# Performance work log

Measured on AMD Instinct MI355X. Metric: run time of the kernel, lower is better.

The kernel has to match this reference:

```python
import jax, jax.numpy as jnp
import numpy as np

B, T = 2, 1024
D_MODEL = 2048
D_STATE = 64            # N
HEADDIM = 64            # P (module sets headdim = d_state)
EXPAND = 2
D_CONV = 4
NGROUPS = 1
D_INNER = EXPAND * D_MODEL                     # 4096
NHEADS = D_INNER // HEADDIM                    # 64
CONV_DIM = D_INNER + 2 * NGROUPS * D_STATE     # 4224
D_IN_PROJ = 2 * D_INNER + 2 * NGROUPS * D_STATE + NHEADS  # 8384
EPS = 1e-5


def setup_inputs() -> dict:
    key = jax.random.key(0)
    k = jax.random.split(key, 10)
    n = lambda kk, sh, sc: jax.random.normal(kk, sh, jnp.float32) * sc
    return {
        "x": n(k[0], (B, T, D_MODEL), 1.0),
        "ln_w": jnp.ones((D_MODEL,), jnp.float32),
        "ln_b": jnp.zeros((D_MODEL,), jnp.float32),
        "in_proj_w": n(k[1], (D_IN_PROJ, D_MODEL), D_MODEL ** -0.5),
        "conv_w": n(k[2], (CONV_DIM, D_CONV), 0.5),
        "conv_b": n(k[3], (CONV_DIM,), 0.02),
        "dt_bias": n(k[4], (NHEADS,), 0.5),
        "A_log": jnp.log(jax.random.uniform(k[5], (NHEADS,), jnp.float32, 1.0, 16.0)),
        "D": 1.0 + n(k[6], (NHEADS,), 0.1),
        "norm_w": jnp.ones((D_INNER,), jnp.float32),
        "out_proj_w": n(k[7], (D_MODEL, D_INNER), D_INNER ** -0.5),
    }


def _layernorm(x, w, b):
    mu = x.mean(-1, keepdims=True)
    var = ((x - mu) ** 2).mean(-1, keepdims=True)
    return (x - mu) * jax.lax.rsqrt(var + EPS) * w + b


def _mamba2(u, in_proj_w, conv_w, conv_b, dt_bias, A_log, D, norm_w, out_proj_w):
    zxbcdt = u @ in_proj_w.T                         # [B,T,D_IN_PROJ]
    z = zxbcdt[..., :D_INNER]                        # gate
    xBC = zxbcdt[..., D_INNER:D_INNER + CONV_DIM]
    dt = zxbcdt[..., D_INNER + CONV_DIM:]            # [B,T,H]
    # causal depthwise conv1d (kernel size D_CONV) + SiLU
    xp = jnp.pad(xBC, ((0, 0), (D_CONV - 1, 0), (0, 0)))
    conv = conv_b
    for kk in range(D_CONV):
        conv = conv + xp[:, kk:kk + T, :] * conv_w[:, kk]
    xBC = jax.nn.silu(conv)
    x_in = xBC[..., :D_INNER].reshape(B, T, NHEADS, HEADDIM)   # [B,T,H,P]
    Bm = xBC[..., D_INNER:D_INNER + D_STATE]         # [B,T,N] (ngroups=1)
    Cm = xBC[..., D_INNER + D_STATE:]                # [B,T,N]
    dt = jax.nn.softplus(dt + dt_bias)               # [B,T,H]
    A = -jnp.exp(A_log)                              # [H]
    dA = jnp.exp(dt * A)                             # [B,T,H]
    dtx = dt[..., None] * x_in                       # [B,T,H,P]

    def step(h, inp):
        dA_t, dtx_t, B_t, C_t = inp
        # h: [B,H,P,N]
        h = h * dA_t[:, :, None, None] + dtx_t[..., None] * B_t[:, None, None, :]
        y = jnp.einsum('bhpn,bn->bhp', h, C_t)
        return h, y

    h0 = jnp.zeros((B, NHEADS, HEADDIM, D_STATE), u.dtype)
    xs = (jnp.moveaxis(dA, 1, 0), jnp.moveaxis(dtx, 1, 0),
          jnp.moveaxis(Bm, 1, 0), jnp.moveaxis(Cm, 1, 0))
    _, ys = jax.lax.scan(step, h0, xs)               # ys: [T,B,H,P]
    y = jnp.moveaxis(ys, 0, 1) + D[:, None] * x_in   # skip term D*x
    y = y.reshape(B, T, D_INNER)
    # gated RMSNorm (norm_before_gate=False): rmsnorm(y * silu(z)) * w
    y = y * jax.nn.silu(z)
    y = y * jax.lax.rsqrt((y * y).mean(-1, keepdims=True) + EPS) * norm_w
    return y @ out_proj_w.T                          # [B,T,D_MODEL]


def reference(x, ln_w, ln_b, in_proj_w, conv_w, conv_b, dt_bias, A_log, D, norm_w, out_proj_w):
    # pre-norm Mamba2 block with residual: x + Mamba2(LayerNorm(x))
    return x + _mamba2(_layernorm(x, ln_w, ln_b), in_proj_w, conv_w, conv_b,
                       dt_bias, A_log, D, norm_w, out_proj_w)
```

## Files before the change

### kernel.cpp

```cpp
#include <hip/hip_runtime.h>
#include <hip/hip_bf16.h>

#define Bdim 2
#define Tdim 1024
#define DMODEL 2048
#define DSTATE 64
#define HEADDIM 64
#define DCONV 4
#define DINNER 4096
#define NHEADS 64
#define CONVDIM 4224
#define DINPROJ 8384
#define NPAD 8448
#define MROWS (Bdim*Tdim)
#define QC 64
#define NCHUNK (Tdim/QC)

typedef __attribute__((ext_vector_type(8))) short bf16x8;
typedef __attribute__((ext_vector_type(4))) float f32x4;
typedef __attribute__((ext_vector_type(4))) unsigned short u16x4;
typedef __attribute__((ext_vector_type(8))) unsigned short u16x8;

#define GLB(p) ((const __attribute__((address_space(1))) void*)(p))
#define LDS(p) ((__attribute__((address_space(3))) void*)(p))

__device__ __forceinline__ unsigned short f2bf(float f) {
    unsigned int x = __builtin_bit_cast(unsigned int, f);
    x += 0x7fffu + ((x >> 16) & 1u);
    return (unsigned short)(x >> 16);
}
__device__ __forceinline__ float bf2f(unsigned int u16) {
    unsigned int x = u16 << 16;
    return __builtin_bit_cast(float, x);
}
__device__ __forceinline__ float siluf(float v) {
    return v / (1.f + expf(-v));
}

#define CVT_A4 (NPAD * DMODEL / 4)
#define CVT_B4 (DMODEL * DINNER / 4)
#define CVT_BLKS ((CVT_A4 + CVT_B4) / 256)
__global__ __launch_bounds__(256) void prep_k(const float* __restrict__ in_proj,
                                              const float* __restrict__ out_proj,
                                              unsigned short* __restrict__ win,
                                              unsigned short* __restrict__ wout,
                                              const float* __restrict__ x,
                                              const float* __restrict__ lw,
                                              const float* __restrict__ lb,
                                              unsigned short* __restrict__ u) {
    if (blockIdx.x < CVT_BLKS) {
        int idx = blockIdx.x * 256 + threadIdx.x;
        if (idx < CVT_A4) {
            int i4 = idx * 4;
            int row = i4 >> 11;
            u16x4 o;
            if (row < DINPROJ) {
                float4 v = *(const float4*)(in_proj + i4);
                o = (u16x4){f2bf(v.x), f2bf(v.y), f2bf(v.z), f2bf(v.w)};
            } else {
                o = (u16x4){0, 0, 0, 0};
            }
            *(u16x4*)(win + i4) = o;
        } else {
            int i4 = (idx - CVT_A4) * 4;
            float4 v = *(const float4*)(out_proj + i4);
            *(u16x4*)(wout + i4) = (u16x4){f2bf(v.x), f2bf(v.y), f2bf(v.z), f2bf(v.w)};
        }
        return;
    }
    int row = blockIdx.x - CVT_BLKS;
    const float* xr = x + (size_t)row * DMODEL;
    float4 v[2];
    float s = 0.f, s2 = 0.f;
#pragma unroll
    for (int i = 0; i < 2; ++i) {
        int c = (threadIdx.x + 256 * i) * 4;
        v[i] = *(const float4*)(xr + c);
        s += v[i].x + v[i].y + v[i].z + v[i].w;
        s2 += v[i].x * v[i].x + v[i].y * v[i].y + v[i].z * v[i].z + v[i].w * v[i].w;
    }
#pragma unroll
    for (int off = 32; off; off >>= 1) { s += __shfl_down(s, off); s2 += __shfl_down(s2, off); }
    __shared__ float rs[4], rs2[4];
    if ((threadIdx.x & 63) == 0) { rs[threadIdx.x >> 6] = s; rs2[threadIdx.x >> 6] = s2; }
    __syncthreads();
    s = rs[0] + rs[1] + rs[2] + rs[3];
    s2 = rs2[0] + rs2[1] + rs2[2] + rs2[3];
    float mu = s * (1.f / DMODEL);
    float var = s2 * (1.f / DMODEL) - mu * mu;
    float inv = rsqrtf(var + 1e-5f);
#pragma unroll
    for (int i = 0; i < 2; ++i) {
        int c = (threadIdx.x + 256 * i) * 4;
        float4 wv = *(const float4*)(lw + c);
        float4 bv = *(const float4*)(lb + c);
        u16x4 o = {f2bf((v[i].x - mu) * inv * wv.x + bv.x),
                   f2bf((v[i].y - mu) * inv * wv.y + bv.y),
                   f2bf((v[i].z - mu) * inv * wv.z + bv.z),
                   f2bf((v[i].w - mu) * inv * wv.w + bv.w)};
        *(u16x4*)(u + (size_t)row * DMODEL + c) = o;
    }
}

#define WAITV(n) asm volatile("s_waitcnt vmcnt(" #n ")" ::: "memory")
#define LGKM0   do { asm volatile("s_waitcnt lgkmcnt(0)" ::: "memory"); \
                     __builtin_amdgcn_sched_barrier(0); } while (0)
#define SCB     __builtin_amdgcn_sched_barrier(0)
#define BAR     __builtin_amdgcn_s_barrier()

template <int KTILES>
__global__ __launch_bounds__(512, 2) void gemm8(const unsigned short* __restrict__ A,
                                                const unsigned short* __restrict__ Bw,
                                                float* __restrict__ Cout,
                                                int N, int lda, int ldb,
                                                int nb, int mb) {
    __shared__ unsigned short As[2][256 * 64];
    __shared__ unsigned short Bs[2][128 * 64];

    const int bid = blockIdx.x;
    const int per_panel = mb * 8;
    const int fullp = (nb / 8) * per_panel;
    int mt, nt;
    if (bid < fullp) {
        int p = bid / per_panel, r = bid % per_panel;
        nt = p * 8 + r / mb; mt = r % mb;
    } else {
        int r = bid - fullp;
        nt = (nb / 8) * 8 + r / mb; mt = r % mb;
    }
    const int m0 = mt * 256, n0 = nt * 128;

    const int tid = threadIdx.x;
    const int lane = tid & 63, w = tid >> 6;
    const int wm = (w >> 1) * 64;
    const int wn = (w & 1) * 64;
    const int row16 = lane & 15, quad = lane >> 4;
    const int swz = row16 & 7;

    const unsigned short* gA[4];
    const unsigned short* gB[2];
#pragma unroll
    for (int l = 0; l < 4; ++l) {
        int c = l * 512 + tid, r = c >> 3, kb = (c & 7) ^ (r & 7);
        gA[l] = A + (size_t)(m0 + r) * lda + kb * 8;
    }
#pragma unroll
    for (int l = 0; l < 2; ++l) {
        int c = l * 512 + tid, r = c >> 3, kb = (c & 7) ^ (r & 7);
        gB[l] = Bw + (size_t)(n0 + r) * ldb + kb * 8;
    }

#define STG_A(d, l, kt) __builtin_amdgcn_global_load_lds(GLB(gA[l] + (kt) * 64), \
                            LDS(&As[d][((l) * 512 + tid) * 8]), 16, 0, 0)
#define STG_B(d, l, kt) __builtin_amdgcn_global_load_lds(GLB(gB[l] + (kt) * 64), \
                            LDS(&Bs[d][((l) * 512 + tid) * 8]), 16, 0, 0)
#define RD_B(d) _Pragma("unroll") for (int j = 0; j < 4; ++j)                      \
                _Pragma("unroll") for (int kc = 0; kc < 2; ++kc) {                 \
                    int row = wn + j * 16 + row16;                                 \
                    int g = (kc * 4 + quad) ^ swz;                                 \
                    bfr[j][kc] = *(const bf16x8*)&Bs[d][(row * 8 + g) * 8];        \
                }
#define RD_A(d, ms) _Pragma("unroll") for (int i2 = 0; i2 < 2; ++i2)               \
                    _Pragma("unroll") for (int kc = 0; kc < 2; ++kc) {             \
                        int row = wm + ((ms) * 2 + i2) * 16 + row16;               \
                        int g = (kc * 4 + quad) ^ swz;                             \
                        af[i2][kc] = *(const bf16x8*)&As[d][(row * 8 + g) * 8];    \
                    }
#define MM(ms) do { __builtin_amdgcn_s_setprio(1);                                  \
                    _Pragma("unroll") for (int kc = 0; kc < 2; ++kc)                \
                    _Pragma("unroll") for (int i2 = 0; i2 < 2; ++i2)                \
                    _Pragma("unroll") for (int j = 0; j < 4; ++j)                   \
                        acc[(ms) * 2 + i2][j] = __builtin_amdgcn_mfma_f32_16x16x32_bf16( \
                            af[i2][kc], bfr[j][kc], acc[(ms) * 2 + i2][j], 0, 0, 0);\
                    __builtin_amdgcn_s_setprio(0); } while (0)

    f32x4 acc[4][4];
#pragma unroll
    for (int i = 0; i < 4; ++i)
#pragma unroll
        for (int j = 0; j < 4; ++j) acc[i][j] = (f32x4){0.f, 0.f, 0.f, 0.f};
    bf16x8 bfr[4][2], af[2][2];

    STG_A(0, 0, 0); STG_A(0, 1, 0); STG_A(0, 2, 0); STG_A(0, 3, 0);
    STG_B(0, 0, 0); STG_B(0, 1, 0);

    const int KI = KTILES / 2;
    for (int i = 0; i < KI; ++i) {
        const int k1 = 2 * i + 1, k2 = 2 * i + 2;
        const bool st2 = (k2 < KTILES);
        STG_A(1, 0, k1); STG_A(1, 1, k1); STG_A(1, 2, k1); STG_A(1, 3, k1);
        WAITV(4);
        BAR;
        RD_B(0); RD_A(0, 0);
        LGKM0;
        MM(0);
        BAR;
        RD_A(0, 1);
        STG_B(1, 0, k1); STG_B(1, 1, k1);
        BAR;
        LGKM0;
        MM(1);
        BAR;
        if (st2) {
            STG_A(0, 0, k2); STG_A(0, 1, k2); STG_A(0, 2, k2); STG_A(0, 3, k2);
            WAITV(4);
        } else {
            WAITV(0);
        }
        BAR;
        RD_B(1); RD_A(1, 0);
        LGKM0;
        MM(0);
        BAR;
        RD_A(1, 1);
        if (st2) { STG_B(0, 0, k2); STG_B(0, 1, k2); }
        BAR;
        LGKM0;
        MM(1);
        BAR;
    }

#pragma unroll
    for (int i2 = 0; i2 < 4; ++i2)
#pragma unroll
        for (int j = 0; j < 4; ++j)
#pragma unroll
            for (int r = 0; r < 4; ++r) {
                int m = m0 + wm + i2 * 16 + quad * 4 + r;
                int n = n0 + wn + j * 16 + row16;
                Cout[(size_t)m * N + n] = acc[i2][j][r];
            }
#undef STG_A
#undef STG_B
#undef RD_A
#undef RD_B
#undef MM
}

template <int EPI, int BM, int BN, int KTILES>
__global__ __launch_bounds__(512, 1) void gemm_mf(const unsigned short* __restrict__ A,
                                                  const unsigned short* __restrict__ Bw,
                                                  float* __restrict__ Cout,
                                                  const float* __restrict__ resid,
                                                  int N, int lda, int ldb,
                                                  int nb, int mb) {
    constexpr int NA = BM / 64;
    constexpr int NB = BN / 64;
    constexpr int IM = BM / 64;
    constexpr int IMH = IM / 2;
    constexpr int IN = BN / 32;

    __shared__ unsigned short As[3][BM * 64];
    __shared__ unsigned short Bs[3][BN * 64];

    const int bid = blockIdx.x;
    const int per_panel = mb * 8;
    const int fullp = (nb / 8) * per_panel;
    int mt, nt;
    if (bid < fullp) {
        int p = bid / per_panel, r = bid % per_panel;
        nt = p * 8 + r / mb; mt = r % mb;
    } else {
        int r = bid - fullp;
        nt = (nb / 8) * 8 + r / mb; mt = r % mb;
    }
    const int m0 = mt * BM, n0 = nt * BN;

    const int tid = threadIdx.x;
    const int lane = tid & 63, w = tid >> 6;
    const int wm = (w >> 1) * (BM / 4);
    const int wn = (w & 1) * 64;
    const int row16 = lane & 15, quad = lane >> 4;
    const int swz = row16 & 7;

    const unsigned short* gA[NA]; int oA[NA];
    const unsigned short* gB[NB]; int oB[NB];
#pragma unroll
    for (int l = 0; l < NA; ++l) {
        int c = l * 512 + tid, r = c >> 3, kb = (c & 7) ^ (r & 7);
        gA[l] = A + (size_t)(m0 + r) * lda + kb * 8;
        oA[l] = c * 8;
    }
#pragma unroll
    for (int l = 0; l < NB; ++l) {
        int c = l * 512 + tid, r = c >> 3, kb = (c & 7) ^ (r & 7);
        gB[l] = Bw + (size_t)(n0 + r) * ldb + kb * 8;
        oB[l] = c * 8;
    }

#define STG_A(d, kt) do { _Pragma("unroll")                                           \
    for (int _l = 0; _l < NA; ++_l)                                                   \
        __builtin_amdgcn_global_load_lds(GLB(gA[_l] + (kt) * 64),                     \
                                         LDS(&As[d][oA[_l]]), 16, 0, 0); } while (0)
#define STG_B(d, kt) do { _Pragma("unroll")                                           \
    for (int _l = 0; _l < NB; ++_l)                                                   \
        __builtin_amdgcn_global_load_lds(GLB(gB[_l] + (kt) * 64),                     \
                                         LDS(&Bs[d][oB[_l]]), 16, 0, 0); } while (0)
#define RD_B(Bb) do { _Pragma("unroll") for (int _j = 0; _j < IN; ++_j)               \
                      _Pragma("unroll") for (int _kc = 0; _kc < 2; ++_kc) {           \
                          int _row = wn + _j * 16 + row16;                            \
                          int _g = (_kc * 4 + quad) ^ swz;                            \
                          bfr[_j][_kc] = *(const bf16x8*)&(Bb)[(_row * 8 + _g) * 8];  \
                      } } while (0)
#define RD_A(Ab, h) do { _Pragma("unroll") for (int _i = 0; _i < IMH; ++_i)           \
                         _Pragma("unroll") for (int _kc = 0; _kc < 2; ++_kc) {        \
                             int _row = wm + ((h) * IMH + _i) * 16 + row16;           \
                             int _g = (_kc * 4 + quad) ^ swz;                         \
                             af[_i][_kc] = *(const bf16x8*)&(Ab)[(_row * 8 + _g) * 8];\
                         } } while (0)
#define MM(h) do { __builtin_amdgcn_s_setprio(1);                                     \
                   _Pragma("unroll") for (int _kc = 0; _kc < 2; ++_kc)                \
                   _Pragma("unroll") for (int _i = 0; _i < IMH; ++_i)                 \
                   _Pragma("unroll") for (int _j = 0; _j < IN; ++_j)                  \
                       acc[(h) * IMH + _i][_j] = __builtin_amdgcn_mfma_f32_16x16x32_bf16( \
                           af[_i][_kc], bfr[_j][_kc], acc[(h) * IMH + _i][_j], 0, 0, 0);  \
                   __builtin_amdgcn_s_setprio(0); } while (0)

    f32x4 acc[IM][IN];
#pragma unroll
    for (int i = 0; i < IM; ++i)
#pragma unroll
        for (int j = 0; j < IN; ++j) acc[i][j] = (f32x4){0.f, 0.f, 0.f, 0.f};
    bf16x8 bfr[IN][2], af[IMH][2];

    STG_A(0, 0); STG_B(0, 0);
    STG_A(1, 1); STG_B(1, 1);
    if constexpr (BM == 256) WAITV(6); else WAITV(4);
    BAR;

    int bc = 0;
    for (int t = 0; t < KTILES; ++t) {
        int bn2 = bc + 2; if (bn2 >= 3) bn2 -= 3;
        const unsigned short* Ab = As[bc];
        const unsigned short* Bb = Bs[bc];
        const bool pf = (t + 2 < KTILES);

        RD_B(Bb); RD_A(Ab, 0);
        if (pf) STG_A(bn2, t + 2);
        SCB;
        BAR;
        LGKM0;
        MM(0);
        BAR;
        RD_A(Ab, 1);
        if (pf) STG_B(bn2, t + 2);
        SCB;
        if (t + 2 < KTILES) { if constexpr (BM == 256) WAITV(6); else WAITV(4); }
        else if (t + 1 < KTILES) WAITV(0);
        BAR;
        LGKM0;
        MM(1);
        BAR;
        bc = bc + 1; if (bc == 3) bc = 0;
    }

#pragma unroll
    for (int i = 0; i < IM; ++i)
#pragma unroll
        for (int j = 0; j < IN; ++j)
#pragma unroll
            for (int r = 0; r < 4; ++r) {
                int m = m0 + wm + i * 16 + quad * 4 + r;
                int n = n0 + wn + j * 16 + row16;
                float v = acc[i][j][r];
                if (EPI == 0)
                    Cout[(size_t)m * N + n] = v;
                else
                    Cout[(size_t)m * N + n] = resid[(size_t)m * N + n] + v;
            }
#undef STG_A
#undef STG_B
#undef RD_A
#undef RD_B
#undef MM
}

#define CONV_T (MROWS * CONVDIM / 4)
__global__ __launch_bounds__(256) void convdt_k(const float* __restrict__ zx,
                                                const float* __restrict__ cw,
                                                const float* __restrict__ cb,
                                                const float* __restrict__ dt_bias,
                                                const float* __restrict__ A_log,
                                                float* __restrict__ xin,
                                                float* __restrict__ bcf,
                                                float* __restrict__ dtf,
                                                float* __restrict__ dtAf) {
    int idx = blockIdx.x * 256 + threadIdx.x;
    if (idx < CONV_T) {
        int cg = idx % (CONVDIM / 4);
        int bt = idx / (CONVDIM / 4);
        int c = cg * 4;
        int t = bt & (Tdim - 1);
        const float* base = zx + (size_t)bt * NPAD + DINNER + c;
        float4 acc = *(const float4*)(cb + c);
#pragma unroll
        for (int kk = 0; kk < DCONV; ++kk) {
            int tt = t - 3 + kk;
            if (tt >= 0) {
                float4 v = *(const float4*)(base + (long)(kk - 3) * NPAD);
                acc.x += v.x * cw[(c + 0) * 4 + kk];
                acc.y += v.y * cw[(c + 1) * 4 + kk];
                acc.z += v.z * cw[(c + 2) * 4 + kk];
                acc.w += v.w * cw[(c + 3) * 4 + kk];
            }
        }
        float4 s = {siluf(acc.x), siluf(acc.y), siluf(acc.z), siluf(acc.w)};
        if (c < DINNER) *(float4*)(xin + (size_t)bt * DINNER + c) = s;
        else            *(float4*)(bcf + (size_t)bt * 128 + (c - DINNER)) = s;
    } else {
        int d4 = (idx - CONV_T) * 4;
        int bt = d4 >> 6;
        int h = d4 & 63;
        float4 raw = *(const float4*)(zx + (size_t)bt * NPAD + (DINNER + CONVDIM) + h);
        float4 bias = *(const float4*)(dt_bias + h);
        float4 al = *(const float4*)(A_log + h);
        float r[4] = {raw.x + bias.x, raw.y + bias.y, raw.z + bias.z, raw.w + bias.w};
        float A[4] = {-expf(al.x), -expf(al.y), -expf(al.z), -expf(al.w)};
        float4 dtv, dta;
        float* dtp = (float*)&dtv; float* dap = (float*)&dta;
#pragma unroll
        for (int j = 0; j < 4; ++j) {
            float dv = (r[j] > 20.f) ? r[j] : log1pf(expf(r[j]));
            dtp[j] = dv;
            dap[j] = dv * A[j];
        }
        *(float4*)(dtf + bt * 64 + h) = dtv;
        *(float4*)(dtAf + bt * 64 + h) = dta;
    }
}

__global__ __launch_bounds__(256) void chunk_state_k(const float* __restrict__ xin,
                                                     const float* __restrict__ bcf,
                                                     const float* __restrict__ dtf,
                                                     const float* __restrict__ dtAf,
                                                     float* __restrict__ Sst,
                                                     float* __restrict__ laq) {
    const int blk = blockIdx.x;
    const int c = blk & 15, h = (blk >> 4) & 63, b = blk >> 10;
    const int bt0 = b * Tdim + c * QC;
    const int tid = threadIdx.x;

    __shared__ float Bs[QC][68];
    __shared__ float Dx[QC][68];
    __shared__ float wsh[QC];

    if (tid < QC) {
        float v = dtAf[(bt0 + tid) * NHEADS + h];
#pragma unroll
        for (int d = 1; d < 64; d <<= 1) {
            float o = __shfl_up(v, d, 64);
            v += (tid >= d) ? o : 0.f;
        }
        float la63 = __shfl(v, 63, 64);
        wsh[tid] = expf(la63 - v);
        if (tid == 63) laq[blk] = la63;
    }
    __syncthreads();

    const int row = tid >> 2, q = tid & 3;
    {
        float m = wsh[row] * dtf[(bt0 + row) * NHEADS + h];
        const float* xr = xin + (size_t)(bt0 + row) * DINNER + h * 64 + q * 16;
        const float* br = bcf + (size_t)(bt0 + row) * 128 + q * 16;
#pragma unroll
        for (int j = 0; j < 4; ++j) {
            float4 xv = *(const float4*)(xr + j * 4);
            float4 bv = *(const float4*)(br + j * 4);
            *(float4*)&Dx[row][q * 16 + j * 4] = (float4){m * xv.x, m * xv.y, m * xv.z, m * xv.w};
            *(float4*)&Bs[row][q * 16 + j * 4] = bv;
        }
    }
    __syncthreads();

    const int p0 = (tid >> 4) * 4, n0 = (tid & 15) * 4;
    float acc[4][4] = {};
    for (int i = 0; i < QC; ++i) {
        float4 dv = *(const float4*)&Dx[i][p0];
        float4 bv = *(const float4*)&Bs[i][n0];
        float dva[4] = {dv.x, dv.y, dv.z, dv.w};
        float bva[4] = {bv.x, bv.y, bv.z, bv.w};
#pragma unroll
        for (int a = 0; a < 4; ++a)
#pragma unroll
            for (int e = 0; e < 4; ++e) acc[a][e] += dva[a] * bva[e];
    }
    float* Sp = Sst + (size_t)blk * NPAD;
#pragma unroll
    for (int a = 0; a < 4; ++a)
        *(float4*)&Sp[(p0 + a) * 64 + n0] = (float4){acc[a][0], acc[a][1], acc[a][2], acc[a][3]};
}

__global__ __launch_bounds__(256) void combine_k(float* __restrict__ Sst,
                                                 const float* __restrict__ laq) {
    const int bh = blockIdx.x >> 1;
    const int half = blockIdx.x & 1;
    const int tid = threadIdx.x;
    float4 r0 = {}, r1 = {};
    for (int c = 0; c < NCHUNK - 1; ++c) {
        float* p = Sst + (size_t)(bh * 16 + c) * NPAD + half * 2048 + tid * 8;
        float P = expf(laq[bh * 16 + c]);
        float4 s0 = ((const float4*)p)[0], s1 = ((const float4*)p)[1];
        r0 = (float4){P * r0.x + s0.x, P * r0.y + s0.y, P * r0.z + s0.z, P * r0.w + s0.w};
        r1 = (float4){P * r1.x + s1.x, P * r1.y + s1.y, P * r1.z + s1.z, P * r1.w + s1.w};
        ((float4*)p)[0] = r0; ((float4*)p)[1] = r1;
    }
}

__global__ __launch_bounds__(256) void chunk_out_k2(float* __restrict__ xin,
                                                    const float* __restrict__ bcf,
                                                    const float* __restrict__ dtf,
                                                    const float* __restrict__ dtAf,
                                                    const float* __restrict__ Sst,
                                                    const float* __restrict__ Dp) {
    const int blk = blockIdx.x;
    const int c = blk & 15, h = (blk >> 4) & 63, b = blk >> 10;
    const int bt0 = b * Tdim + c * QC;
    const int tid = threadIdx.x;

    __shared__ unsigned short Csh[64 * 64];
    __shared__ unsigned short Bsh[64 * 64];
    __shared__ unsigned short DxT[64 * 64];
    __shared__ unsigned short Gh [64 * 64];
    __shared__ unsigned short Hh [64 * 64];
    __shared__ float lash[QC];

    if (tid < QC) {
        float v = dtAf[(bt0 + tid) * NHEADS + h];
#pragma unroll
        for (int d = 1; d < 64; d <<= 1) {
            float o = __shfl_up(v, d, 64);
            v += (tid >= d) ? o : 0.f;
        }
        lash[tid] = v;
    }

    const int row = tid >> 2, q = tid & 3;
    {
        float m = dtf[(bt0 + row) * NHEADS + h];
        const float* xr = xin + (size_t)(bt0 + row) * DINNER + h * 64 + q * 16;
        const float* br = bcf + (size_t)(bt0 + row) * 128 + q * 16;
        const float* cr = bcf + (size_t)(bt0 + row) * 128 + 64 + q * 16;
        float xb[16];
        u16x8 cc[2], bb[2];
#pragma unroll
        for (int j = 0; j < 4; ++j) {
            float4 xv = *(const float4*)(xr + j * 4);
            float4 bv = *(const float4*)(br + j * 4);
            float4 cv = *(const float4*)(cr + j * 4);
            xb[j * 4 + 0] = m * xv.x; xb[j * 4 + 1] = m * xv.y;
            xb[j * 4 + 2] = m * xv.z; xb[j * 4 + 3] = m * xv.w;
            int hi = j >> 1, lo = (j & 1) * 4;
            cc[hi][lo + 0] = f2bf(cv.x); cc[hi][lo + 1] = f2bf(cv.y);
            cc[hi][lo + 2] = f2bf(cv.z); cc[hi][lo + 3] = f2bf(cv.w);
            bb[hi][lo + 0] = f2bf(bv.x); bb[hi][lo + 1] = f2bf(bv.y);
            bb[hi][lo + 2] = f2bf(bv.z); bb[hi][lo + 3] = f2bf(bv.w);
        }
        const int base = row * 64;
        const int c0 = ((q * 2) ^ (row & 7)) * 8, c1 = ((q * 2 + 1) ^ (row & 7)) * 8;
        *(u16x8*)&Csh[base + c0] = cc[0];  *(u16x8*)&Csh[base + c1] = cc[1];
        *(u16x8*)&Bsh[base + c0] = bb[0];  *(u16x8*)&Bsh[base + c1] = bb[1];
#pragma unroll
        for (int k2 = 0; k2 < 16; ++k2) {
            int p = q * 16 + k2;
            DxT[p * 64 + (((row >> 3) ^ (p & 7)) * 8 + (row & 7))] = f2bf(xb[k2]);
        }
        if (c > 0) {
            const float* Hp = Sst + (size_t)(blk - 1) * NPAD + row * 64 + q * 16;
            u16x8 hh[2];
#pragma unroll
            for (int j = 0; j < 4; ++j) {
                float4 hv = *(const float4*)(Hp + j * 4);
                int hi = j >> 1, lo = (j & 1) * 4;
                hh[hi][lo + 0] = f2bf(hv.x); hh[hi][lo + 1] = f2bf(hv.y);
                hh[hi][lo + 2] = f2bf(hv.z); hh[hi][lo + 3] = f2bf(hv.w);
            }
            *(u16x8*)&Hh[base + c0] = hh[0];  *(u16x8*)&Hh[base + c1] = hh[1];
        }
    }
    __syncthreads();

    const int lane = tid & 63, w = tid >> 6;
    const int t0 = w * 16;
    const int row16 = lane & 15, quad = lane >> 4;
    const int swz = row16 & 7;

    f32x4 a1[4];
#pragma unroll
    for (int st = 0; st < 4; ++st) a1[st] = (f32x4){0.f, 0.f, 0.f, 0.f};
#pragma unroll
    for (int kc = 0; kc < 2; ++kc) {
        int g = ((kc * 4 + quad) ^ swz) * 8;
        bf16x8 ca = *(const bf16x8*)&Csh[(t0 + row16) * 64 + g];
#pragma unroll
        for (int st = 0; st < 4; ++st) {
            bf16x8 bs = *(const bf16x8*)&Bsh[(st * 16 + row16) * 64 + g];
            a1[st] = __builtin_amdgcn_mfma_f32_16x16x32_bf16(ca, bs, a1[st], 0, 0, 0);
        }
    }
    float latv[4];
#pragma unroll
    for (int r = 0; r < 4; ++r) latv[r] = lash[t0 + quad * 4 + r];
#pragma unroll
    for (int st = 0; st < 4; ++st) {
        int s = st * 16 + row16;
        float las = lash[s];
#pragma unroll
        for (int r = 0; r < 4; ++r) {
            int t = t0 + quad * 4 + r;
            float gv = (s <= t) ? a1[st][r] * expf(latv[r] - las) : 0.f;
            Gh[t * 64 + (((s >> 3) ^ (t & 7)) * 8 + (s & 7))] = f2bf(gv);
        }
    }
    __syncthreads();

    f32x4 aS[4], aH[4];
#pragma unroll
    for (int pt = 0; pt < 4; ++pt) { aS[pt] = (f32x4){0.f,0.f,0.f,0.f}; aH[pt] = (f32x4){0.f,0.f,0.f,0.f}; }
#pragma unroll
    for (int kc = 0; kc < 2; ++kc) {
        int g = ((kc * 4 + quad) ^ swz) * 8;
        bf16x8 ga = *(const bf16x8*)&Gh[(t0 + row16) * 64 + g];
#pragma unroll
        for (int pt = 0; pt < 4; ++pt) {
            bf16x8 db = *(const bf16x8*)&DxT[(pt * 16 + row16) * 64 + g];
            aS[pt] = __builtin_amdgcn_mfma_f32_16x16x32_bf16(ga, db, aS[pt], 0, 0, 0);
        }
        if (c > 0) {
            bf16x8 ca = *(const bf16x8*)&Csh[(t0 + row16) * 64 + g];
#pragma unroll
            for (int pt = 0; pt < 4; ++pt) {
                bf16x8 hb = *(const bf16x8*)&Hh[(pt * 16 + row16) * 64 + g];
                aH[pt] = __builtin_amdgcn_mfma_f32_16x16x32_bf16(ca, hb, aH[pt], 0, 0, 0);
            }
        }
    }

    float Dh = Dp[h];
    float eA[4];
#pragma unroll
    for (int r = 0; r < 4; ++r) eA[r] = expf(latv[r]);
#pragma unroll
    for (int pt = 0; pt < 4; ++pt)
#pragma unroll
        for (int r = 0; r < 4; ++r) {
            int t = t0 + quad * 4 + r, p = pt * 16 + row16;
            float* xr2 = xin + (size_t)(bt0 + t) * DINNER + h * 64 + p;
            float xv = *xr2;
            float y = aS[pt][r] + Dh * xv;
            if (c > 0) y += eA[r] * aH[pt][r];
            *xr2 = y;
        }
}

__global__ __launch_bounds__(256) void gate_k(const float* __restrict__ ybf,
                                              const float* __restrict__ zx,
                                              const float* __restrict__ nw,
                                              unsigned short* __restrict__ yg,
                                              int ldyg) {
    int row = blockIdx.x;
    float4 tv[4];
    float s2 = 0.f;
#pragma unroll
    for (int i = 0; i < 4; ++i) {
        int c = (threadIdx.x + 256 * i) * 4;
        float4 y = *(const float4*)(ybf + (size_t)row * DINNER + c);
        float4 z = *(const float4*)(zx + (size_t)row * NPAD + c);
        float4 t = {y.x * siluf(z.x), y.y * siluf(z.y), y.z * siluf(z.z), y.w * siluf(z.w)};
        tv[i] = t;
        s2 += t.x * t.x + t.y * t.y + t.z * t.z + t.w * t.w;
    }
#pragma unroll
    for (int off = 32; off; off >>= 1) s2 += __shfl_down(s2, off);
    __shared__ float rs[4];
    if ((threadIdx.x & 63) == 0) rs[threadIdx.x >> 6] = s2;
    __syncthreads();
    s2 = rs[0] + rs[1] + rs[2] + rs[3];
    float scale = rsqrtf(s2 * (1.f / DINNER) + 1e-5f);
#pragma unroll
    for (int i = 0; i < 4; ++i) {
        int c = (threadIdx.x + 256 * i) * 4;
        float4 w = *(const float4*)(nw + c);
        u16x4 o = {f2bf(tv[i].x * scale * w.x), f2bf(tv[i].y * scale * w.y),
                   f2bf(tv[i].z * scale * w.z), f2bf(tv[i].w * scale * w.w)};
        *(u16x4*)(yg + (size_t)row * ldyg + c) = o;
    }
}

extern "C" void kernel_launch(void* const* d_in, const int* in_sizes, int n_in,
                              void* d_out, int out_size, void* d_ws, size_t ws_size,
                              hipStream_t stream) {
    const float* x        = (const float*)d_in[0];
    const float* ln_w     = (const float*)d_in[1];
    const float* ln_b     = (const float*)d_in[2];
    const float* in_proj  = (const float*)d_in[3];
    const float* conv_w   = (const float*)d_in[4];
    const float* conv_b   = (const float*)d_in[5];
    const float* dt_bias  = (const float*)d_in[6];
    const float* A_log    = (const float*)d_in[7];
    const float* Dp       = (const float*)d_in[8];
    const float* norm_w   = (const float*)d_in[9];
    const float* out_proj = (const float*)d_in[10];
    float* out = (float*)d_out;
    char* ws = (char*)d_ws;

    float*          zx   = (float*)(ws + 0);
    unsigned short* wout = (unsigned short*)(ws + 69206016);
    unsigned short* win  = (unsigned short*)(ws + 85983232);
    unsigned short* ubf  = (unsigned short*)(ws + 120586240);
    float*          xin  = (float*)(ws + 85983232);
    float*          bcf  = (float*)(ws + 120586240);
    float*          dtf  = (float*)(ws + 121634816);
    float*          dtAf = (float*)(ws + 122159104);
    float*          laq  = (float*)(ws + 122683392);
    float*          Sst  = zx + 4096;
    unsigned short* yg   = (unsigned short*)zx + 8192;
    const int       ldyg = 16896;

    prep_k<<<CVT_BLKS + MROWS, 256, 0, stream>>>(in_proj, out_proj, win, wout,
                                                 x, ln_w, ln_b, ubf);
    gemm8<32><<<66 * 8, 512, 0, stream>>>(ubf, win, zx, NPAD, DMODEL, DMODEL, 66, 8);
    convdt_k<<<(CONV_T + MROWS * NHEADS / 4) / 256, 256, 0, stream>>>(zx, conv_w, conv_b,
                                                                      dt_bias, A_log,
                                                                      xin, bcf, dtf, dtAf);
    chunk_state_k<<<Bdim * NHEADS * NCHUNK, 256, 0, stream>>>(xin, bcf, dtf, dtAf, Sst, laq);
    combine_k<<<2 * Bdim * NHEADS, 256, 0, stream>>>(Sst, laq);
    chunk_out_k2<<<Bdim * NHEADS * NCHUNK, 256, 0, stream>>>(xin, bcf, dtf, dtAf, Sst, Dp);
    gate_k<<<MROWS, 256, 0, stream>>>(xin, zx, norm_w, yg, ldyg);
    gemm_mf<1, 128, 128, 64><<<16 * 16, 512, 0, stream>>>(yg, wout, out, x,
                                                          DMODEL, ldyg, DINNER, 16, 16);
}
```

Before: 466.3 us.

## Unify GEMMs into double-buffered template with smaller tiles and higher occupancy

Replaces the fixed 256x128 in-projection GEMM and the triple-buffered out-projection GEMM with one templated double-buffered kernel that uses launch_bounds(512,4). The in-projection now runs with 128x128 tiles (twice the blocks) and the out-projection with 128x64 tiles (twice the blocks). This is meant to improve CU fill and occupancy on both GEMMs. In exchange each block reuses less data per tile, and the pipeline depth of the out-projection drops from three buffers to two.

```diff
diff --git a/kernel.cpp b/kernel.cpp
--- a/kernel.cpp
+++ b/kernel.cpp
@@ -108,14 +108,21 @@
 #define SCB     __builtin_amdgcn_sched_barrier(0)
 #define BAR     __builtin_amdgcn_s_barrier()
 
-template <int KTILES>
-__global__ __launch_bounds__(512, 2) void gemm8(const unsigned short* __restrict__ A,
-                                                const unsigned short* __restrict__ Bw,
-                                                float* __restrict__ Cout,
-                                                int N, int lda, int ldb,
-                                                int nb, int mb) {
-    __shared__ unsigned short As[2][256 * 64];
-    __shared__ unsigned short Bs[2][128 * 64];
+template <int EPI, int BM, int BN, int KTILES>
+__global__ __launch_bounds__(512, 4) void gemm_cr(const unsigned short* __restrict__ A,
+                                                  const unsigned short* __restrict__ Bw,
+                                                  float* __restrict__ Cout,
+                                                  const float* __restrict__ resid,
+                                                  int N, int lda, int ldb,
+                                                  int nb, int mb) {
+    constexpr int NA = BM / 64;
+    constexpr int NB = BN / 64;
+    constexpr int IM = BM / 64;
+    constexpr int IMH = IM / 2;
+    constexpr int IN = BN / 32;
+
+    __shared__ unsigned short As[2][BM * 64];
+    __shared__ unsigned short Bs[2][BN * 64];
 
     const int bid = blockIdx.x;
     const int per_panel = mb * 8;
@@ -128,186 +135,49 @@
         int r = bid - fullp;
         nt = (nb / 8) * 8 + r / mb; mt = r % mb;
     }
-    const int m0 = mt * 256, n0 = nt * 128;
-
-    const int tid = threadIdx.x;
-    const int lane = tid & 63, w = tid >> 6;
-    const int wm = (w >> 1) * 64;
-    const int wn = (w & 1) * 64;
-    const int row16 = lane & 15, quad = lane >> 4;
-    const int swz = row16 & 7;
-
-    const unsigned short* gA[4];
-    const unsigned short* gB[2];
-#pragma unroll
-    for (int l = 0; l < 4; ++l) {
-        int c = l * 512 + tid, r = c >> 3, kb = (c & 7) ^ (r & 7);
-        gA[l] = A + (size_t)(m0 + r) * lda + kb * 8;
-    }
-#pragma unroll
-    for (int l = 0; l < 2; ++l) {
-        int c = l * 512 + tid, r = c >> 3, kb = (c & 7) ^ (r & 7);
-        gB[l] = Bw + (size_t)(n0 + r) * ldb + kb * 8;
-    }
-
-#define STG_A(d, l, kt) __builtin_amdgcn_global_load_lds(GLB(gA[l] + (kt) * 64), \
-                            LDS(&As[d][((l) * 512 + tid) * 8]), 16, 0, 0)
-#define STG_B(d, l, kt) __builtin_amdgcn_global_load_lds(GLB(gB[l] + (kt) * 64), \
-                            LDS(&Bs[d][((l) * 512 + tid) * 8]), 16, 0, 0)
-#define RD_B(d) _Pragma("unroll") for (int j = 0; j < 4; ++j)                      \
-                _Pragma("unroll") for (int kc = 0; kc < 2; ++kc) {                 \
-                    int row = wn + j * 16 + row16;                                 \
-                    int g = (kc * 4 + quad) ^ swz;                                 \
-                    bfr[j][kc] = *(const bf16x8*)&Bs[d][(row * 8 + g) * 8];        \
-                }
-#define RD_A(d, ms) _Pragma("unroll") for (int i2 = 0; i2 < 2; ++i2)               \
-                    _Pragma("unroll") for (int kc = 0; kc < 2; ++kc) {             \
-                        int row = wm + ((ms) * 2 + i2) * 16 + row16;               \
-                        int g = (kc * 4 + quad) ^ swz;                             \
-                        af[i2][kc] = *(const bf16x8*)&As[d][(row * 8 + g) * 8];    \
-                    }
-#define MM(ms) do { __builtin_amdgcn_s_setprio(1);                                  \
-                    _Pragma("unroll") for (int kc = 0; kc < 2; ++kc)                \
-                    _Pragma("unroll") for (int i2 = 0; i2 < 2; ++i2)                \
-                    _Pragma("unroll") for (int j = 0; j < 4; ++j)                   \
-                        acc[(ms) * 2 + i2][j] = __builtin_amdgcn_mfma_f32_16x16x32_bf16( \
-                            af[i2][kc], bfr[j][kc], acc[(ms) * 2 + i2][j], 0, 0, 0);\
-                    __builtin_amdgcn_s_setprio(0); } while (0)
-
-    f32x4 acc[4][4];
-#pragma unroll
-    for (int i = 0; i < 4; ++i)
-#pragma unroll
-        for (int j = 0; j < 4; ++j) acc[i][j] = (f32x4){0.f, 0.f, 0.f, 0.f};
-    bf16x8 bfr[4][2], af[2][2];
-
-    STG_A(0, 0, 0); STG_A(0, 1, 0); STG_A(0, 2, 0); STG_A(0, 3, 0);
-    STG_B(0, 0, 0); STG_B(0, 1, 0);
-
-    const int KI = KTILES / 2;
-    for (int i = 0; i < KI; ++i) {
-        const int k1 = 2 * i + 1, k2 = 2 * i + 2;
-        const bool st2 = (k2 < KTILES);
-        STG_A(1, 0, k1); STG_A(1, 1, k1); STG_A(1, 2, k1); STG_A(1, 3, k1);
-        WAITV(4);
-        BAR;
-        RD_B(0); RD_A(0, 0);
-        LGKM0;
-        MM(0);
-        BAR;
-        RD_A(0, 1);
-        STG_B(1, 0, k1); STG_B(1, 1, k1);
-        BAR;
-        LGKM0;
-        MM(1);
-        BAR;
-        if (st2) {
-            STG_A(0, 0, k2); STG_A(0, 1, k2); STG_A(0, 2, k2); STG_A(0, 3, k2);
-            WAITV(4);
-        } else {
-            WAITV(0);
-        }
-        BAR;
-        RD_B(1); RD_A(1, 0);
-        LGKM0;
-        MM(0);
-        BAR;
-        RD_A(1, 1);
-        if (st2) { STG_B(0, 0, k2); STG_B(0, 1, k2); }
-        BAR;
-        LGKM0;
-        MM(1);
-        BAR;
-    }
-
-#pragma unroll
-    for (int i2 = 0; i2 < 4; ++i2)
-#pragma unroll
-        for (int j = 0; j < 4; ++j)
-#pragma unroll
-            for (int r = 0; r < 4; ++r) {
-                int m = m0 + wm + i2 * 16 + quad * 4 + r;
-                int n = n0 + wn + j * 16 + row16;
-                Cout[(size_t)m * N + n] = acc[i2][j][r];
-            }
-#undef STG_A
-#undef STG_B
-#undef RD_A
-#undef RD_B
-#undef MM
-}
-
-template <int EPI, int BM, int BN, int KTILES>
-__global__ __launch_bounds__(512, 1) void gemm_mf(const unsigned short* __restrict__ A,
-                                                  const unsigned short* __restrict__ Bw,
-                                                  float* __restrict__ Cout,
-                                                  const float* __restrict__ resid,
-                                                  int N, int lda, int ldb,
-                                                  int nb, int mb) {
-    constexpr int NA = BM / 64;
-    constexpr int NB = BN / 64;
-    constexpr int IM = BM / 64;
-    constexpr int IMH = IM / 2;
-    constexpr int IN = BN / 32;
-
-    __shared__ unsigned short As[3][BM * 64];
-    __shared__ unsigned short Bs[3][BN * 64];
-
-    const int bid = blockIdx.x;
-    const int per_panel = mb * 8;
-    const int fullp = (nb / 8) * per_panel;
-    int mt, nt;
-    if (bid < fullp) {
-        int p = bid / per_panel, r = bid % per_panel;
-        nt = p * 8 + r / mb; mt = r % mb;
-    } else {
-        int r = bid - fullp;
-        nt = (nb / 8) * 8 + r / mb; mt = r % mb;
-    }
     const int m0 = mt * BM, n0 = nt * BN;
 
     const int tid = threadIdx.x;
     const int lane = tid & 63, w = tid >> 6;
     const int wm = (w >> 1) * (BM / 4);
-    const int wn = (w & 1) * 64;
+    const int wn = (w & 1) * (BN / 2);
     const int row16 = lane & 15, quad = lane >> 4;
     const int swz = row16 & 7;
 
-    const unsigned short* gA[NA]; int oA[NA];
-    const unsigned short* gB[NB]; int oB[NB];
+    const unsigned short* gA[NA];
+    const unsigned short* gB[NB];
 #pragma unroll
     for (int l = 0; l < NA; ++l) {
         int c = l * 512 + tid, r = c >> 3, kb = (c & 7) ^ (r & 7);
         gA[l] = A + (size_t)(m0 + r) * lda + kb * 8;
-        oA[l] = c * 8;
     }
 #pragma unroll
     for (int l = 0; l < NB; ++l) {
         int c = l * 512 + tid, r = c >> 3, kb = (c & 7) ^ (r & 7);
         gB[l] = Bw + (size_t)(n0 + r) * ldb + kb * 8;
-        oB[l] = c * 8;
     }
 
 #define STG_A(d, kt) do { _Pragma("unroll")                                           \
     for (int _l = 0; _l < NA; ++_l)                                                   \
         __builtin_amdgcn_global_load_lds(GLB(gA[_l] + (kt) * 64),                     \
-                                         LDS(&As[d][oA[_l]]), 16, 0, 0); } while (0)
+                LDS(&As[d][(_l * 512 + tid) * 8]), 16, 0, 0); } while (0)
 #define STG_B(d, kt) do { _Pragma("unroll")                                           \
     for (int _l = 0; _l < NB; ++_l)                                                   \
         __builtin_amdgcn_global_load_lds(GLB(gB[_l] + (kt) * 64),                     \
-                                         LDS(&Bs[d][oB[_l]]), 16, 0, 0); } while (0)
-#define RD_B(Bb) do { _Pragma("unroll") for (int _j = 0; _j < IN; ++_j)               \
-                      _Pragma("unroll") for (int _kc = 0; _kc < 2; ++_kc) {           \
-                          int _row = wn + _j * 16 + row16;                            \
-                          int _g = (_kc * 4 + quad) ^ swz;                            \
-                          bfr[_j][_kc] = *(const bf16x8*)&(Bb)[(_row * 8 + _g) * 8];  \
-                      } } while (0)
-#define RD_A(Ab, h) do { _Pragma("unroll") for (int _i = 0; _i < IMH; ++_i)           \
-                         _Pragma("unroll") for (int _kc = 0; _kc < 2; ++_kc) {        \
-                             int _row = wm + ((h) * IMH + _i) * 16 + row16;           \
-                             int _g = (_kc * 4 + quad) ^ swz;                         \
-                             af[_i][_kc] = *(const bf16x8*)&(Ab)[(_row * 8 + _g) * 8];\
-                         } } while (0)
+                LDS(&Bs[d][(_l * 512 + tid) * 8]), 16, 0, 0); } while (0)
+#define WAITN() do { if constexpr (NA == 2) WAITV(2); else WAITV(4); } while (0)
+#define RD_B(d) do { _Pragma("unroll") for (int _j = 0; _j < IN; ++_j)                \
+                     _Pragma("unroll") for (int _kc = 0; _kc < 2; ++_kc) {            \
+                         int _row = wn + _j * 16 + row16;                             \
+                         int _g = (_kc * 4 + quad) ^ swz;                             \
+                         bfr[_j][_kc] = *(const bf16x8*)&Bs[d][(_row * 8 + _g) * 8];  \
+                     } } while (0)
+#define RD_A(d, h) do { _Pragma("unroll") for (int _i = 0; _i < IMH; ++_i)            \
+                        _Pragma("unroll") for (int _kc = 0; _kc < 2; ++_kc) {         \
+                            int _row = wm + ((h) * IMH + _i) * 16 + row16;            \
+                            int _g = (_kc * 4 + quad) ^ swz;                          \
+                            af[_i][_kc] = *(const bf16x8*)&As[d][(_row * 8 + _g) * 8];\
+                        } } while (0)
 #define MM(h) do { __builtin_amdgcn_s_setprio(1);                                     \
                    _Pragma("unroll") for (int _kc = 0; _kc < 2; ++_kc)                \
                    _Pragma("unroll") for (int _i = 0; _i < IMH; ++_i)                 \
@@ -324,34 +194,41 @@
     bf16x8 bfr[IN][2], af[IMH][2];
 
     STG_A(0, 0); STG_B(0, 0);
-    STG_A(1, 1); STG_B(1, 1);
-    if constexpr (BM == 256) WAITV(6); else WAITV(4);
-    BAR;
-
-    int bc = 0;
-    for (int t = 0; t < KTILES; ++t) {
-        int bn2 = bc + 2; if (bn2 >= 3) bn2 -= 3;
-        const unsigned short* Ab = As[bc];
-        const unsigned short* Bb = Bs[bc];
-        const bool pf = (t + 2 < KTILES);
-
-        RD_B(Bb); RD_A(Ab, 0);
-        if (pf) STG_A(bn2, t + 2);
-        SCB;
-        BAR;
+
+    const int KI = KTILES / 2;
+    for (int i = 0; i < KI; ++i) {
+        const int k1 = 2 * i + 1, k2 = 2 * i + 2;
+        const bool st2 = (k2 < KTILES);
+        STG_A(1, k1);
+        WAITN();
+        BAR;
+        RD_B(0); RD_A(0, 0);
         LGKM0;
         MM(0);
         BAR;
-        RD_A(Ab, 1);
-        if (pf) STG_B(bn2, t + 2);
-        SCB;
-        if (t + 2 < KTILES) { if constexpr (BM == 256) WAITV(6); else WAITV(4); }
-        else if (t + 1 < KTILES) WAITV(0);
+        RD_A(0, 1);
+        STG_B(1, k1);
         BAR;
         LGKM0;
         MM(1);
         BAR;
-        bc = bc + 1; if (bc == 3) bc = 0;
+        if (st2) {
+            STG_A(0, k2);
+            WAITN();
+        } else {
+            WAITV(0);
+        }
+        BAR;
+        RD_B(1); RD_A(1, 0);
+        LGKM0;
+        MM(0);
+        BAR;
+        RD_A(1, 1);
+        if (st2) STG_B(0, k2);
+        BAR;
+        LGKM0;
+        MM(1);
+        BAR;
     }
 
 #pragma unroll
@@ -370,6 +247,7 @@
             }
 #undef STG_A
 #undef STG_B
+#undef WAITN
 #undef RD_A
 #undef RD_B
 #undef MM
@@ -718,7 +596,8 @@
 
     prep_k<<<CVT_BLKS + MROWS, 256, 0, stream>>>(in_proj, out_proj, win, wout,
                                                  x, ln_w, ln_b, ubf);
-    gemm8<32><<<66 * 8, 512, 0, stream>>>(ubf, win, zx, NPAD, DMODEL, DMODEL, 66, 8);
+    gemm_cr<0, 128, 128, 32><<<66 * 16, 512, 0, stream>>>(ubf, win, zx, nullptr,
+                                                          NPAD, DMODEL, DMODEL, 66, 16);
     convdt_k<<<(CONV_T + MROWS * NHEADS / 4) / 256, 256, 0, stream>>>(zx, conv_w, conv_b,
                                                                       dt_bias, A_log,
                                                                       xin, bcf, dtf, dtAf);
@@ -726,6 +605,6 @@
     combine_k<<<2 * Bdim * NHEADS, 256, 0, stream>>>(Sst, laq);
     chunk_out_k2<<<Bdim * NHEADS * NCHUNK, 256, 0, stream>>>(xin, bcf, dtf, dtAf, Sst, Dp);
     gate_k<<<MROWS, 256, 0, stream>>>(xin, zx, norm_w, yg, ldyg);
-    gemm_mf<1, 128, 128, 64><<<16 * 16, 512, 0, stream>>>(yg, wout, out, x,
-                                                          DMODEL, ldyg, DINNER, 16, 16);
-}
+    gemm_cr<1, 128, 64, 64><<<32 * 16, 512, 0, stream>>>(yg, wout, out, x,
+                                                         DMODEL, ldyg, DINNER, 32, 16);
+}
```

Measured after the change: 428.1 us. 1.09x faster.
